# Kernel optimization log

Hardware: AMD Instinct MI355X
Metric: run time of the kernel (lower is better)

## Reference

```python
import jax, jax.numpy as jnp
import numpy as np

MARGIN = 0.3
N = 8192
D = 128
NUM_CLASSES = 256

def setup_inputs() -> dict:
    key = jax.random.key(0)
    k1, k2 = jax.random.split(key)
    inputs = jax.random.normal(k1, (N, D), dtype=jnp.float32)
    targets = jax.random.randint(k2, (N,), 0, NUM_CLASSES, dtype=jnp.int64)
    return {"inputs": inputs, "targets": targets}

def reference(inputs, targets):
    n = inputs.shape[0]
    dt = inputs.dtype
    # pairwise euclidean distances: ||xi||^2 + ||xj||^2 - 2 xi.xj, clamped and sqrt'ed
    sq = jnp.sum(inputs * inputs, axis=1)                     # [n]
    d2 = sq[:, None] + sq[None, :] - 2.0 * (inputs @ inputs.T)
    dist = jnp.sqrt(jnp.clip(d2, 1e-12, None))                # [n, n]
    dsq = dist * dist                                         # squared dists used by the loss

    mask = targets[:, None] == targets[None, :]               # same-identity mask [n, n]

    # positives: torch code sorts and drops the smallest (the self-distance ~1e-6)
    pos_d = jnp.where(mask, dist, jnp.inf)
    min_idx = jnp.argmin(pos_d, axis=1)                       # index of dropped element per row
    excl = jnp.arange(n)[None, :] == min_idx[:, None]
    pos_valid = mask & ~excl                                  # remaining positives
    cnt_p = jnp.sum(pos_valid, axis=1).astype(dt)
    sigma_p = jnp.sum(jnp.where(pos_valid, dsq, 0.0), axis=1) / cnt_p
    max_p = jnp.max(jnp.where(pos_valid, dsq, -jnp.inf), axis=1)
    dist_ap = max_p / sigma_p + 0.5 * jnp.log(sigma_p)        # [n]

    # negatives: all different-identity entries
    neg = ~mask
    cnt_n = jnp.sum(neg, axis=1).astype(dt)
    sigma_n = jnp.sum(jnp.where(neg, dsq, 0.0), axis=1) / cnt_n
    min_n = jnp.min(jnp.where(neg, dsq, jnp.inf), axis=1)
    dist_an = min_n / sigma_n + 0.5 * jnp.log(sigma_n)        # [n]

    # MarginRankingLoss with y=1: mean(max(0, -(an - ap) + margin))
    loss = jnp.mean(jnp.maximum(dist_ap - dist_an + MARGIN, 0.0))
    return loss
```

## Files before the change

### kernel.cpp

```cpp
#include <hip/hip_runtime.h>
#include <math.h>


#define NROWS 8192
#define MARGIN_F 0.3f

typedef short bf16x8 __attribute__((ext_vector_type(8)));
typedef float f32x16 __attribute__((ext_vector_type(16)));
union U4B { uint4 u; bf16x8 h; };

__device__ __forceinline__ unsigned short f2bf(float x) {
    unsigned u = __float_as_uint(x);
    return (unsigned short)((u + 0x7fffu + ((u >> 16) & 1u)) >> 16);
}

__global__ __launch_bounds__(256) void histscan_kernel(const int* __restrict__ tgt,
                                                       int* __restrict__ hist,
                                                       int* __restrict__ cstart,
                                                       int* __restrict__ coffset,
                                                       float* __restrict__ S_class,
                                                       int* __restrict__ done) {
    __shared__ int h[256];
    __shared__ int wsum[4];
    int t = threadIdx.x;
    h[t] = 0;
    S_class[t] = 0.0f;
    if (t == 0) *done = 0;
    __syncthreads();
    for (int i = t; i < NROWS; i += 256) atomicAdd(&h[tgt[i]], 1);
    __syncthreads();
    int hv = h[t];
    hist[t] = hv;
    int x = hv;
    #pragma unroll
    for (int d = 1; d < 64; d <<= 1) {
        int y = __shfl_up(x, d, 64);
        if ((t & 63) >= d) x += y;
    }
    if ((t & 63) == 63) wsum[t >> 6] = x;
    __syncthreads();
    int off = 0;
    for (int i = 0; i < (t >> 6); ++i) off += wsum[i];
    int excl = off + x - hv;
    cstart[t] = excl;
    coffset[t] = excl;
    if (t == 255) cstart[256] = NROWS;
}

__global__ __launch_bounds__(256) void prep_kernel(const float* __restrict__ X,
                                                   const int* __restrict__ tgt,
                                                   float* __restrict__ sq,
                                                   float* __restrict__ upk,
                                                   unsigned short* __restrict__ Xbf,
                                                   int* __restrict__ coffset,
                                                   float* __restrict__ S_class,
                                                   float* __restrict__ bsum) {
    int tid = threadIdx.x, w = tid >> 6, l = tid & 63;
    int row0 = blockIdx.x * 32 + w * 8;
    float rs = 0.0f;
    #pragma unroll
    for (int i = 0; i < 8; ++i) {
        int r = row0 + i;
        float2 v = ((const float2*)X)[(size_t)r * 64 + l];
        ushort2 h2;
        h2.x = f2bf(v.x);
        h2.y = f2bf(v.y);
        float s = v.x * v.x + v.y * v.y;
        for (int d = 32; d > 0; d >>= 1) s += __shfl_down(s, d, 64);
        int pos = 0;
        if (l == 0) {
            int c = tgt[r];
            pos = atomicAdd(&coffset[c], 1);
            sq[pos] = s;
            rs += s;
            upk[pos] = __uint_as_float((__float_as_uint(0.5f * s) & 0xffffff00u) | (unsigned)c);
            atomicAdd(&S_class[c], s);
        }
        pos = __shfl(pos, 0, 64);
        ((ushort2*)Xbf)[(size_t)pos * 64 + l] = h2;
    }
    __shared__ float bs[4];
    if (l == 0) bs[w] = rs;
    __syncthreads();
    if (tid == 0) bsum[blockIdx.x] = bs[0] + bs[1] + bs[2] + bs[3];
}

__global__ __launch_bounds__(256, 2) void dist_kernel(
        const unsigned short* __restrict__ Xbf, const float* __restrict__ upk,
        const int* __restrict__ cstart, float4* __restrict__ partial,
        int ns_mask, int jb_shift, int tiles) {
    __shared__ uint4 As[2][2048];
    const int tid = threadIdx.x;
    const int w = tid >> 6, l = tid & 63, hl = l >> 5, l31 = l & 31;
    const int bx = blockIdx.x;
    const int slice = bx & ns_mask;
    const int jb = bx >> jb_shift;
    const int col0 = jb * 64;

    {
        const uint4* srcb = (const uint4*)Xbf + (size_t)col0 * 16;
        #pragma unroll
        for (int s = 0; s < 4; ++s) {
            int L = s * 256 + tid;
            int si = (L & ~15) | ((L & 15) ^ ((L >> 4) & 15));
            __builtin_amdgcn_global_load_lds(
                (const __attribute__((address_space(1))) unsigned int*)(srcb + si),
                (__attribute__((address_space(3))) unsigned int*)(&As[1][s * 256 + w * 64]),
                16, 0, 0);
        }
    }
    const int row_base = slice * tiles * 128;
    {
        const uint4* srca = (const uint4*)Xbf + (size_t)row_base * 16;
        #pragma unroll
        for (int s = 0; s < 8; ++s) {
            int L = s * 256 + tid;
            int si = (L & ~15) | ((L & 15) ^ ((L >> 4) & 15));
            __builtin_amdgcn_global_load_lds(
                (const __attribute__((address_space(1))) unsigned int*)(srca + si),
                (__attribute__((address_space(3))) unsigned int*)(&As[0][s * 256 + w * 64]),
                16, 0, 0);
        }
    }
    const int c_first = __float_as_int(upk[col0]) & 0xff;
    const int c_last  = __float_as_int(upk[col0 + 63]) & 0xff;
    const int U0 = cstart[c_first];
    const int U1 = cstart[c_last + 1];
    int tjt[2];
    tjt[0] = __float_as_int(upk[col0 + l31]) & 0xff;
    tjt[1] = __float_as_int(upk[col0 + 32 + l31]) & 0xff;
    __syncthreads();

    bf16x8 Bf[2][8];
    #pragma unroll
    for (int ct = 0; ct < 2; ++ct) {
        int colb = ct * 32 + l31;
        #pragma unroll
        for (int kk = 0; kk < 8; ++kk) {
            U4B tb; tb.u = As[1][colb * 16 + ((kk * 2 + hl) ^ (colb & 15))];
            Bf[ct][kk] = tb.h;
        }
    }
    __syncthreads();

    float Sa[2] = {0.f, 0.f};
    float Ss[2] = {0.f, 0.f};
    float Mp[2] = {-INFINITY, -INFINITY};
    float Mn[2] = { INFINITY,  INFINITY};
    const int arow = w * 32 + l31;

    for (int t = 0; t < tiles; ++t) {
        const int i0 = row_base + t * 128;

        if (t + 1 < tiles) {
            const uint4* srca = (const uint4*)Xbf + (size_t)(i0 + 128) * 16;
            uint4* dst = As[(t + 1) & 1];
            #pragma unroll
            for (int s = 0; s < 8; ++s) {
                int L = s * 256 + tid;
                int si = (L & ~15) | ((L & 15) ^ ((L >> 4) & 15));
                __builtin_amdgcn_global_load_lds(
                    (const __attribute__((address_space(1))) unsigned int*)(srca + si),
                    (__attribute__((address_space(3))) unsigned int*)(dst + s * 256 + w * 64),
                    16, 0, 0);
            }
        }

        float ur[16];
        const float4* up = (const float4*)(upk + i0 + w * 32 + 4 * hl);
        #pragma unroll
        for (int g = 0; g < 4; ++g) {
            float4 u4 = up[g * 2];
            ur[g * 4 + 0] = u4.x; ur[g * 4 + 1] = u4.y;
            ur[g * 4 + 2] = u4.z; ur[g * 4 + 3] = u4.w;
        }

        const uint4* cur = As[t & 1];
        f32x16 acc[2];
        acc[0] = (f32x16)0.0f;
        acc[1] = (f32x16)0.0f;
        #pragma unroll
        for (int kk = 0; kk < 8; ++kk) {
            U4B a; a.u = cur[arow * 16 + ((kk * 2 + hl) ^ (arow & 15))];
            acc[0] = __builtin_amdgcn_mfma_f32_32x32x16_bf16(a.h, Bf[0][kk], acc[0], 0, 0, 0);
            acc[1] = __builtin_amdgcn_mfma_f32_32x32x16_bf16(a.h, Bf[1][kk], acc[1], 0, 0, 0);
        }

        if (i0 < U1 && i0 + 128 > U0) {
            #pragma unroll
            for (int ct = 0; ct < 2; ++ct) {
                const int tt = tjt[ct];
                #pragma unroll
                for (int r = 0; r < 16; ++r) {
                    float a = acc[ct][r];
                    float v = ur[r] - a;
                    bool same = ((__float_as_int(ur[r]) & 0xff) == tt);
                    Sa[ct] += a;
                    Ss[ct] += same ? a : 0.0f;
                    Mp[ct] = fmaxf(Mp[ct], same ? v : -INFINITY);
                    Mn[ct] = same ? Mn[ct] : fminf(Mn[ct], v);
                }
            }
        } else {
            #pragma unroll
            for (int ct = 0; ct < 2; ++ct) {
                #pragma unroll
                for (int r = 0; r < 16; ++r) {
                    float a = acc[ct][r];
                    Sa[ct] += a;
                    Mn[ct] = fminf(Mn[ct], ur[r] - a);
                }
            }
        }
        __syncthreads();
    }

    #pragma unroll
    for (int ct = 0; ct < 2; ++ct) {
        Sa[ct] += __shfl_xor(Sa[ct], 32, 64);
        Ss[ct] += __shfl_xor(Ss[ct], 32, 64);
        Mp[ct] = fmaxf(Mp[ct], __shfl_xor(Mp[ct], 32, 64));
        Mn[ct] = fminf(Mn[ct], __shfl_xor(Mn[ct], 32, 64));
    }
    float4* sm = (float4*)&As[0][0];
    if (l < 32) {
        #pragma unroll
        for (int ct = 0; ct < 2; ++ct)
            sm[(ct * 32 + l31) * 4 + w] = make_float4(Sa[ct], Ss[ct], Mp[ct], Mn[ct]);
    }
    __syncthreads();
    if (tid < 64) {
        float4 a = sm[tid * 4 + 0], b = sm[tid * 4 + 1];
        float4 c2 = sm[tid * 4 + 2], d = sm[tid * 4 + 3];
        float4 o;
        o.x = a.x + b.x + c2.x + d.x;
        o.y = a.y + b.y + c2.y + d.y;
        o.z = fmaxf(fmaxf(a.z, b.z), fmaxf(c2.z, d.z));
        o.w = fminf(fminf(a.w, b.w), fminf(c2.w, d.w));
        partial[(size_t)slice * NROWS + col0 + tid] = o;
    }
}

__global__ __launch_bounds__(256) void combine_kernel(
        const float* __restrict__ sq, const float* __restrict__ upk,
        const int* __restrict__ hist, const float* __restrict__ S_class,
        const float* __restrict__ bsum, const float4* __restrict__ partial,
        float* __restrict__ blocksum, int* __restrict__ done,
        float* __restrict__ out, int ns) {
    __shared__ float red[4];
    __shared__ float hs[4];
    __shared__ int lastflag;
    int tid = threadIdx.x, l = tid & 63, w = tid >> 6;

    float b = bsum[tid];
    for (int d = 32; d > 0; d >>= 1) b += __shfl_down(b, d, 64);
    if (l == 0) red[w] = b;
    __syncthreads();
    float S_all = red[0] + red[1] + red[2] + red[3];

    int j = blockIdx.x * 256 + tid;
    float Sa = 0.f, Ss = 0.f, Mp = -INFINITY, Mn = INFINITY;
    for (int s = 0; s < ns; ++s) {
        float4 p = partial[(size_t)s * NROWS + j];
        Sa += p.x; Ss += p.y;
        Mp = fmaxf(Mp, p.z); Mn = fminf(Mn, p.w);
    }
    float sqj = sq[j];
    int c = __float_as_int(upk[j]) & 0xff;
    float cnt = (float)hist[c];
    float sumall = (float)NROWS * sqj + S_all - 2.0f * Sa;
    float sump = cnt * sqj + S_class[c] - 2.0f * Ss;
    float sumn = sumall - sump;
    float sigp = sump / (cnt - 1.0f);
    float sign_ = sumn / ((float)NROWS - cnt);
    float ap = (sqj + 2.0f * Mp) / sigp + 0.5f * __logf(sigp);
    float an = (sqj + 2.0f * Mn) / sign_ + 0.5f * __logf(sign_);
    float h = fmaxf(ap - an + MARGIN_F, 0.0f);
    for (int d = 32; d > 0; d >>= 1) h += __shfl_down(h, d, 64);
    if (l == 0) hs[w] = h;
    __syncthreads();
    if (tid == 0) {
        float tot = hs[0] + hs[1] + hs[2] + hs[3];
        __hip_atomic_store(&blocksum[blockIdx.x], tot,
                           __ATOMIC_RELEASE, __HIP_MEMORY_SCOPE_AGENT);
        int prev = __hip_atomic_fetch_add(done, 1,
                                          __ATOMIC_ACQ_REL, __HIP_MEMORY_SCOPE_AGENT);
        lastflag = (prev == 31) ? 1 : 0;
    }
    __syncthreads();
    if (lastflag) {
        float s2 = 0.0f;
        if (tid < 32)
            s2 = __hip_atomic_load(&blocksum[tid],
                                   __ATOMIC_ACQUIRE, __HIP_MEMORY_SCOPE_AGENT);
        if (tid < 64) {
            for (int d = 32; d > 0; d >>= 1) s2 += __shfl_down(s2, d, 64);
            if (tid == 0) out[0] = s2 * (1.0f / NROWS);
        }
    }
}

extern "C" void kernel_launch(void* const* d_in, const int* in_sizes, int n_in,
                              void* d_out, int out_size, void* d_ws, size_t ws_size,
                              hipStream_t stream) {
    const float* X = (const float*)d_in[0];
    const int* tgt = (const int*)d_in[1];
    float* out = (float*)d_out;

    float* f = (float*)d_ws;
    int*   hist     = (int*)f;
    float* S_class  = f + 256;
    float* bsum     = f + 512;
    float* blocksum = f + 768;
    int*   cstart   = (int*)(f + 800);
    int*   coffset  = (int*)(f + 1088);
    int*   done     = (int*)(f + 1344);
    float* sq       = f + 2048;
    float* upk      = f + 10240;
    unsigned short* Xbf = (unsigned short*)(f + 18432);
    float4* partial = (float4*)(f + 542720);

    int ns = 8;
    while (ns > 2 && ws_size < ((size_t)542720 + (size_t)ns * NROWS * 4) * sizeof(float))
        ns >>= 1;
    int shift = (ns == 8) ? 3 : (ns == 4) ? 2 : 1;
    int tiles = 64 / ns;

    histscan_kernel<<<1, 256, 0, stream>>>(tgt, hist, cstart, coffset, S_class, done);
    prep_kernel<<<256, 256, 0, stream>>>(X, tgt, sq, upk, Xbf, coffset, S_class, bsum);
    dist_kernel<<<128 * ns, 256, 0, stream>>>(Xbf, upk, cstart, partial,
                                              ns - 1, shift, tiles);
    combine_kernel<<<32, 256, 0, stream>>>(sq, upk, hist, S_class, bsum,
                                           partial, blocksum, done, out, ns);
}
```

Measured before the change: 113.7 us.

## Store bf16 rows in MFMA-fragment order and load A/B directly from global

The prep kernel now writes the bf16 copy of X in a tiled layout grouped by 32-row blocks, so each lane's MFMA operand is one contiguous 16-byte load. The distance kernel drops the double-buffered LDS staging and its barriers, reading A and B fragments straight from global memory (relying on L2/cache reuse). The histogram kernel also reads targets as int4. This removes LDS traffic and synchronization, but loses explicit prefetch overlap and exposes global load latency inside the MFMA loop.

```diff
diff --git a/kernel.cpp b/kernel.cpp
--- a/kernel.cpp
+++ b/kernel.cpp
@@ -27,7 +27,14 @@
     S_class[t] = 0.0f;
     if (t == 0) *done = 0;
     __syncthreads();
-    for (int i = t; i < NROWS; i += 256) atomicAdd(&h[tgt[i]], 1);
+    const int4* t4 = (const int4*)tgt;
+    for (int i = t; i < NROWS / 4; i += 256) {
+        int4 v = t4[i];
+        atomicAdd(&h[v.x], 1);
+        atomicAdd(&h[v.y], 1);
+        atomicAdd(&h[v.z], 1);
+        atomicAdd(&h[v.w], 1);
+    }
     __syncthreads();
     int hv = h[t];
     hist[t] = hv;
@@ -77,7 +84,8 @@
             atomicAdd(&S_class[c], s);
         }
         pos = __shfl(pos, 0, 64);
-        ((ushort2*)Xbf)[(size_t)pos * 64 + l] = h2;
+        int g = pos >> 5, rr = pos & 31;
+        ((ushort2*)Xbf)[((size_t)(g * 16 + (l >> 2)) * 32 + rr) * 4 + (l & 3)] = h2;
     }
     __shared__ float bs[4];
     if (l == 0) bs[w] = rs;
@@ -89,82 +97,41 @@
         const unsigned short* __restrict__ Xbf, const float* __restrict__ upk,
         const int* __restrict__ cstart, float4* __restrict__ partial,
         int ns_mask, int jb_shift, int tiles) {
-    __shared__ uint4 As[2][2048];
+    __shared__ float4 sm[64 * 4];
     const int tid = threadIdx.x;
     const int w = tid >> 6, l = tid & 63, hl = l >> 5, l31 = l & 31;
     const int bx = blockIdx.x;
     const int slice = bx & ns_mask;
     const int jb = bx >> jb_shift;
     const int col0 = jb * 64;
-
-    {
-        const uint4* srcb = (const uint4*)Xbf + (size_t)col0 * 16;
+    const uint4* Xq = (const uint4*)Xbf;
+
+    bf16x8 Bf[2][8];
+    #pragma unroll
+    for (int ct = 0; ct < 2; ++ct) {
+        const uint4* bp = Xq + (size_t)(jb * 2 + ct) * 512 + hl * 32 + l31;
         #pragma unroll
-        for (int s = 0; s < 4; ++s) {
-            int L = s * 256 + tid;
-            int si = (L & ~15) | ((L & 15) ^ ((L >> 4) & 15));
-            __builtin_amdgcn_global_load_lds(
-                (const __attribute__((address_space(1))) unsigned int*)(srcb + si),
-                (__attribute__((address_space(3))) unsigned int*)(&As[1][s * 256 + w * 64]),
-                16, 0, 0);
-        }
-    }
-    const int row_base = slice * tiles * 128;
-    {
-        const uint4* srca = (const uint4*)Xbf + (size_t)row_base * 16;
-        #pragma unroll
-        for (int s = 0; s < 8; ++s) {
-            int L = s * 256 + tid;
-            int si = (L & ~15) | ((L & 15) ^ ((L >> 4) & 15));
-            __builtin_amdgcn_global_load_lds(
-                (const __attribute__((address_space(1))) unsigned int*)(srca + si),
-                (__attribute__((address_space(3))) unsigned int*)(&As[0][s * 256 + w * 64]),
-                16, 0, 0);
-        }
-    }
+        for (int kk = 0; kk < 8; ++kk) {
+            U4B tb; tb.u = bp[kk * 64];
+            Bf[ct][kk] = tb.h;
+        }
+    }
+    int tjt[2];
+    tjt[0] = __float_as_int(upk[col0 + l31]) & 0xff;
+    tjt[1] = __float_as_int(upk[col0 + 32 + l31]) & 0xff;
     const int c_first = __float_as_int(upk[col0]) & 0xff;
     const int c_last  = __float_as_int(upk[col0 + 63]) & 0xff;
     const int U0 = cstart[c_first];
     const int U1 = cstart[c_last + 1];
-    int tjt[2];
-    tjt[0] = __float_as_int(upk[col0 + l31]) & 0xff;
-    tjt[1] = __float_as_int(upk[col0 + 32 + l31]) & 0xff;
-    __syncthreads();
-
-    bf16x8 Bf[2][8];
-    #pragma unroll
-    for (int ct = 0; ct < 2; ++ct) {
-        int colb = ct * 32 + l31;
-        #pragma unroll
-        for (int kk = 0; kk < 8; ++kk) {
-            U4B tb; tb.u = As[1][colb * 16 + ((kk * 2 + hl) ^ (colb & 15))];
-            Bf[ct][kk] = tb.h;
-        }
-    }
-    __syncthreads();
 
     float Sa[2] = {0.f, 0.f};
     float Ss[2] = {0.f, 0.f};
     float Mp[2] = {-INFINITY, -INFINITY};
     float Mn[2] = { INFINITY,  INFINITY};
-    const int arow = w * 32 + l31;
+    const int row_base = slice * tiles * 128;
 
     for (int t = 0; t < tiles; ++t) {
         const int i0 = row_base + t * 128;
-
-        if (t + 1 < tiles) {
-            const uint4* srca = (const uint4*)Xbf + (size_t)(i0 + 128) * 16;
-            uint4* dst = As[(t + 1) & 1];
-            #pragma unroll
-            for (int s = 0; s < 8; ++s) {
-                int L = s * 256 + tid;
-                int si = (L & ~15) | ((L & 15) ^ ((L >> 4) & 15));
-                __builtin_amdgcn_global_load_lds(
-                    (const __attribute__((address_space(1))) unsigned int*)(srca + si),
-                    (__attribute__((address_space(3))) unsigned int*)(dst + s * 256 + w * 64),
-                    16, 0, 0);
-            }
-        }
 
         float ur[16];
         const float4* up = (const float4*)(upk + i0 + w * 32 + 4 * hl);
@@ -175,13 +142,13 @@
             ur[g * 4 + 2] = u4.z; ur[g * 4 + 3] = u4.w;
         }
 
-        const uint4* cur = As[t & 1];
+        const uint4* ap = Xq + ((size_t)(i0 >> 5) + w) * 512 + hl * 32 + l31;
         f32x16 acc[2];
         acc[0] = (f32x16)0.0f;
         acc[1] = (f32x16)0.0f;
         #pragma unroll
         for (int kk = 0; kk < 8; ++kk) {
-            U4B a; a.u = cur[arow * 16 + ((kk * 2 + hl) ^ (arow & 15))];
+            U4B a; a.u = ap[kk * 64];
             acc[0] = __builtin_amdgcn_mfma_f32_32x32x16_bf16(a.h, Bf[0][kk], acc[0], 0, 0, 0);
             acc[1] = __builtin_amdgcn_mfma_f32_32x32x16_bf16(a.h, Bf[1][kk], acc[1], 0, 0, 0);
         }
@@ -212,7 +179,6 @@
                 }
             }
         }
-        __syncthreads();
     }
 
     #pragma unroll
@@ -222,7 +188,6 @@
         Mp[ct] = fmaxf(Mp[ct], __shfl_xor(Mp[ct], 32, 64));
         Mn[ct] = fminf(Mn[ct], __shfl_xor(Mn[ct], 32, 64));
     }
-    float4* sm = (float4*)&As[0][0];
     if (l < 32) {
         #pragma unroll
         for (int ct = 0; ct < 2; ++ct)
```

Measured after the change: 107.0 us. 1.06x faster.
